# Performance work log

Measured on AMD Instinct MI355X. Metric: run time of the kernel, lower is better.

Reference implementation:

```python
import jax, jax.numpy as jnp
import numpy as np

T = 8          # message-passing steps (hparams['T'])
D = 64         # link_state_dim
R = 128        # readout_units
E = 100000     # num edges (rows of link_state)
M = 400000     # num messages (len of states_first/second)
G = 1000       # num graphs in the batch


def _gru_cell(x, h, W, U, b):
    """Keras GRUCell with reset_after=True. x:[N,in], h:[N,units].
    W:[in,3u], U:[u,3u], b:[2,3u] (input bias, recurrent bias)."""
    mx = x @ W + b[0]
    mh = h @ U + b[1]
    xz, xr, xh = jnp.split(mx, 3, axis=-1)
    hz, hr, hh = jnp.split(mh, 3, axis=-1)
    z = jax.nn.sigmoid(xz + hz)
    r = jax.nn.sigmoid(xr + hr)
    cand = jnp.tanh(xh + r * hh)
    return z * h + (1.0 - z) * cand


def setup_inputs() -> dict:
    key = jax.random.key(0)
    ks = jax.random.split(key, 12)
    glorot = jax.nn.initializers.glorot_uniform()
    inp = {
        "link_state": jax.random.normal(ks[0], (E, D), jnp.float32),
        "states_first": jax.random.randint(ks[1], (M,), 0, E, jnp.int32),
        "states_second": jax.random.randint(ks[2], (M,), 0, E, jnp.int32),
        "states_graph_ids": jnp.sort(jax.random.randint(ks[3], (E,), 0, G, jnp.int32)),
        "num_edges": E,
        # Message MLP: Dense(D) with selu on concat [*, 2D]
        "W_msg": glorot(ks[4], (2 * D, D), jnp.float32),
        "b_msg": jnp.zeros((D,), jnp.float32),
        # Update GRUCell (units=D, input dim=D)
        "W_upd": glorot(ks[5], (D, 3 * D), jnp.float32),
        "U_upd": glorot(ks[6], (D, 3 * D), jnp.float32),
        "b_upd": jnp.zeros((2, 3 * D), jnp.float32),
        # Readout GRU (units=R, input dim=D)
        "W_ro": glorot(ks[7], (D, 3 * R), jnp.float32),
        "U_ro": glorot(ks[8], (R, 3 * R), jnp.float32),
        "b_ro": jnp.zeros((2, 3 * R), jnp.float32),
        # Final Dense(1)
        "W_out": glorot(ks[9], (R, 1), jnp.float32),
        "b_out": jnp.zeros((1,), jnp.float32),
    }
    return inp


def reference(link_state, states_first, states_second, states_graph_ids, num_edges,
              W_msg, b_msg, W_upd, U_upd, b_upd, W_ro, U_ro, b_ro, W_out, b_out):
    def mp_step(h, _):
        # gather sender/receiver states, concat -> message MLP (selu)
        edges_concat = jnp.concatenate([h[states_first], h[states_second]], axis=1)  # [M, 2D]
        msg = jax.nn.selu(edges_concat @ W_msg + b_msg)                              # [M, D]
        # scatter-add messages to receiver edges
        agg = jax.ops.segment_sum(msg, states_second, num_segments=num_edges)        # [E, D]
        h_new = _gru_cell(agg, h, W_upd, U_upd, b_upd)                               # [E, D]
        return h_new, h_new

    _, seq = jax.lax.scan(mp_step, link_state, None, length=T)  # seq: [T, E, D]

    # Readout GRU over the T-step state sequence per edge; return last hidden state
    def ro_step(h, x_t):
        h_new = _gru_cell(x_t, h, W_ro, U_ro, b_ro)
        return h_new, None

    h0 = jnp.zeros((link_state.shape[0], R), link_state.dtype)
    historial, _ = jax.lax.scan(ro_step, h0, seq)               # [E, R]

    # sorted segment_sum over graph ids, then Dense(1)
    per_graph = jax.ops.segment_sum(historial, states_graph_ids, num_segments=G,
                                    indices_are_sorted=True)    # [G, R]
    return per_graph @ W_out + b_out                             # [G, 1]
```

## Files before the change

kernel.cpp:

```cpp
#include <hip/hip_runtime.h>
#include <hip/hip_bf16.h>

#define D 64
#define R 128
#define NSTEPS 8
#define SELU_SCALE 1.0507009873554805f
#define SELU_ALPHA 1.6732632423543772f
#define PADH 72

typedef _Float16 half8 __attribute__((ext_vector_type(8)));
typedef float f32x4 __attribute__((ext_vector_type(4)));

__device__ __forceinline__ float fast_sig(float x) {
    return __fdividef(1.0f, 1.0f + __expf(-x));
}
__device__ __forceinline__ float fast_tanh(float x) {
    float xc = fminf(fmaxf(x, -15.0f), 15.0f);
    float e = __expf(2.0f * xc);
    return 1.0f - __fdividef(2.0f, e + 1.0f);
}

__global__ __launch_bounds__(256) void swizzle_all(
    const float* __restrict__ Wm, const float* __restrict__ Wu,
    const float* __restrict__ Uu, const float* __restrict__ Wr,
    const float* __restrict__ Ur,
    _Float16* __restrict__ wWm, _Float16* __restrict__ wWu,
    _Float16* __restrict__ wUu, _Float16* __restrict__ wWr,
    _Float16* __restrict__ wUr)
{
    const float* src; _Float16* dst; int K, N;
    switch (blockIdx.y) {
        case 0: src = Wm; dst = wWm; K = 128; N = 64;  break;
        case 1: src = Wu; dst = wWu; K = 64;  N = 192; break;
        case 2: src = Uu; dst = wUu; K = 64;  N = 192; break;
        case 3: src = Wr; dst = wWr; K = 64;  N = 384; break;
        default: src = Ur; dst = wUr; K = 128; N = 384; break;
    }
    int idx = blockIdx.x * 256 + threadIdx.x;
    int KT = K >> 5;
    int total = KT * (N >> 4) * 512;
    if (idx >= total) return;
    int j = idx & 7;
    int lane = (idx >> 3) & 63;
    int kt = (idx >> 9) % KT;
    int nt = idx / (512 * KT);
    int k = 32 * kt + 8 * (lane >> 4) + j;
    int n = 16 * nt + (lane & 15);
    dst[idx] = (_Float16)src[(size_t)k * N + n];
}

__global__ __launch_bounds__(256) void h16_init(const float* __restrict__ src,
                                                _Float16* __restrict__ dst, int n) {
    int i = blockIdx.x * 256 + threadIdx.x;
    if (i < n) dst[i] = (_Float16)src[i];
}

__global__ __launch_bounds__(256) void hist_kernel(const int* __restrict__ second,
                                                   int* __restrict__ cnt, int M) {
    int m = blockIdx.x * 256 + threadIdx.x;
    if (m < M) atomicAdd(&cnt[second[m]], 1);
}

__global__ __launch_bounds__(256) void scan_bsum(const int* __restrict__ cnt,
                                                 int* __restrict__ bsum, int E) {
    int i = blockIdx.x * 256 + threadIdx.x;
    int tid = threadIdx.x;
    int v = (i < E) ? cnt[i] : 0;
    __shared__ int s[256];
    s[tid] = v;
    __syncthreads();
    #pragma unroll
    for (int d = 1; d < 256; d <<= 1) {
        int t = (tid >= d) ? s[tid - d] : 0;
        __syncthreads();
        s[tid] += t;
        __syncthreads();
    }
    if (tid == 255) bsum[blockIdx.x] = s[255];
}

__global__ __launch_bounds__(1024) void scan_part(int* __restrict__ bsum, int NB) {
    int tid = threadIdx.x;
    __shared__ int s[1024];
    int v = (tid < NB) ? bsum[tid] : 0;
    s[tid] = v;
    __syncthreads();
    #pragma unroll
    for (int d = 1; d < 1024; d <<= 1) {
        int t = (tid >= d) ? s[tid - d] : 0;
        __syncthreads();
        s[tid] += t;
        __syncthreads();
    }
    if (tid < NB) bsum[tid] = s[tid] - v;
}

__global__ __launch_bounds__(256) void scan_final(const int* __restrict__ cnt,
                                                  const int* __restrict__ bsum,
                                                  int* __restrict__ off, int E) {
    int i = blockIdx.x * 256 + threadIdx.x;
    int tid = threadIdx.x;
    int v = (i < E) ? cnt[i] : 0;
    __shared__ int s[256];
    s[tid] = v;
    __syncthreads();
    #pragma unroll
    for (int d = 1; d < 256; d <<= 1) {
        int t = (tid >= d) ? s[tid - d] : 0;
        __syncthreads();
        s[tid] += t;
        __syncthreads();
    }
    if (i < E) off[i] = bsum[blockIdx.x] + s[tid] - v;
}

__global__ __launch_bounds__(256) void scatter_kernel(const int* __restrict__ second,
                                                      const int* __restrict__ off,
                                                      int* __restrict__ cur,
                                                      int* __restrict__ perm, int M) {
    int m = blockIdx.x * 256 + threadIdx.x;
    if (m < M) {
        int s = second[m];
        int p = atomicAdd(&cur[s], 1);
        perm[off[s] + p] = m;
    }
}

__global__ __launch_bounds__(256) void fs_pack(const int* __restrict__ first,
                                               const int* __restrict__ second,
                                               const int* __restrict__ perm,
                                               int2* __restrict__ fs, int M) {
    int m = blockIdx.x * 256 + threadIdx.x;
    if (m < M) {
        int pm = perm[m];
        fs[m] = make_int2(first[pm], second[pm]);
    }
}

__global__ __launch_bounds__(256) void step_fused(
    const _Float16* __restrict__ hin,
    _Float16* __restrict__ hout,
    _Float16* hro,
    const int2* __restrict__ fs,
    const int* __restrict__ off,
    const half8* __restrict__ wBm,
    const float* __restrict__ bm,
    const half8* __restrict__ wWu,
    const half8* __restrict__ wUu,
    const float* __restrict__ bu,
    const half8* __restrict__ wWr,
    const half8* __restrict__ wUr,
    const float* __restrict__ br,
    int E, int M)
{
    __shared__ _Float16 smem[4][2][16 * PADH];
    __shared__ int skeys[4][16];

    const int wid = threadIdx.x >> 6;
    const int lane = threadIdx.x & 63;
    const int hi = lane >> 4;
    const int l15 = lane & 15;
    const int e0 = (blockIdx.x * 4 + wid) * 16;

    _Float16* stageH = smem[wid][0];
    _Float16* aggH = smem[wid][1];
    int* skey = skeys[wid];

    {
        unsigned int* az = (unsigned int*)aggH;
        #pragma unroll
        for (int i = 0; i < 9; ++i) az[i * 64 + lane] = 0u;
    }

    half8 Bm[4][4];
    #pragma unroll
    for (int nt = 0; nt < 4; ++nt)
        #pragma unroll
        for (int kt = 0; kt < 4; ++kt)
            Bm[nt][kt] = wBm[(nt * 4 + kt) * 64 + lane];

    if (e0 < E) {
        int b = min(e0 + 16, E);
        int mstart = off[e0];
        int mend = (b == E) ? M : off[b];

        #pragma unroll 1
        for (int ch = 0; mstart + ch * 16 < mend; ++ch) {
            int mrow = mstart + ch * 16 + l15;
            bool mv = (mrow < mend);
            int mcl = min(mrow, mend - 1);
            int2 p = fs[mcl];
            const half8* fr = reinterpret_cast<const half8*>(hin + (size_t)p.x * D);
            const half8* sr = reinterpret_cast<const half8*>(hin + (size_t)p.y * D);
            half8 A[4];
            A[0] = fr[hi];
            A[1] = fr[4 + hi];
            A[2] = sr[hi];
            A[3] = sr[4 + hi];

            f32x4 acc[4];
            #pragma unroll
            for (int nt = 0; nt < 4; ++nt) acc[nt] = (f32x4){0.f, 0.f, 0.f, 0.f};
            #pragma unroll
            for (int nt = 0; nt < 4; ++nt)
                #pragma unroll
                for (int kt = 0; kt < 4; ++kt)
                    acc[nt] = __builtin_amdgcn_mfma_f32_16x16x32_f16(A[kt], Bm[nt][kt], acc[nt], 0, 0, 0);

            #pragma unroll
            for (int nt = 0; nt < 4; ++nt) {
                int n = nt * 16 + l15;
                float bias = bm[n];
                #pragma unroll
                for (int r = 0; r < 4; ++r) {
                    float v = acc[nt][r] + bias;
                    v = (v > 0.0f) ? (SELU_SCALE * v)
                                   : (SELU_SCALE * SELU_ALPHA) * (__expf(v) - 1.0f);
                    stageH[(hi * 4 + r) * PADH + n] = (_Float16)v;
                }
            }
            if (lane < 16) skey[lane] = mv ? (p.y - e0) : -1;

            _Float16 run = (_Float16)0.0f;
            int kprev = skey[0];
            #pragma unroll
            for (int m = 0; m < 16; ++m) {
                int km = skey[m];
                if (km != kprev) {
                    if (kprev >= 0) aggH[kprev * PADH + lane] += run;
                    run = (_Float16)0.0f;
                    kprev = km;
                }
                run += stageH[m * PADH + lane];
            }
            if (kprev >= 0) aggH[kprev * PADH + lane] += run;
        }
    }

    const int ec = min(e0 + l15, E - 1);

    half8 AX[2], AHu[2], AHro[4];
    #pragma unroll
    for (int kt = 0; kt < 2; ++kt) {
        AX[kt] = *reinterpret_cast<const half8*>(&aggH[l15 * PADH + 32 * kt + 8 * hi]);
        AHu[kt] = reinterpret_cast<const half8*>(hin + (size_t)ec * D)[4 * kt + hi];
    }
    #pragma unroll
    for (int kt = 0; kt < 4; ++kt)
        AHro[kt] = reinterpret_cast<const half8*>(hro + (size_t)ec * R)[4 * kt + hi];

    #pragma unroll 1
    for (int i = 0; i < 4; ++i) {
        half8 WBz[2], WBr[2], WBc[2], UBz[2], UBr[2], UBc[2];
        #pragma unroll
        for (int kt = 0; kt < 2; ++kt) {
            WBz[kt] = wWu[((0 + i) * 2 + kt) * 64 + lane];
            WBr[kt] = wWu[((4 + i) * 2 + kt) * 64 + lane];
            WBc[kt] = wWu[((8 + i) * 2 + kt) * 64 + lane];
            UBz[kt] = wUu[((0 + i) * 2 + kt) * 64 + lane];
            UBr[kt] = wUu[((4 + i) * 2 + kt) * 64 + lane];
            UBc[kt] = wUu[((8 + i) * 2 + kt) * 64 + lane];
        }
        int n = 16 * i + l15;
        float bz  = bu[n] + bu[192 + n];
        float brr = bu[64 + n] + bu[256 + n];
        float bx  = bu[128 + n];
        float bh  = bu[320 + n];

        f32x4 az  = (f32x4){0.f, 0.f, 0.f, 0.f};
        f32x4 ar_ = (f32x4){0.f, 0.f, 0.f, 0.f};
        f32x4 acx = (f32x4){0.f, 0.f, 0.f, 0.f};
        f32x4 ach = (f32x4){0.f, 0.f, 0.f, 0.f};
        #pragma unroll
        for (int kt = 0; kt < 2; ++kt) {
            az  = __builtin_amdgcn_mfma_f32_16x16x32_f16(AX[kt], WBz[kt], az, 0, 0, 0);
            az  = __builtin_amdgcn_mfma_f32_16x16x32_f16(AHu[kt], UBz[kt], az, 0, 0, 0);
            ar_ = __builtin_amdgcn_mfma_f32_16x16x32_f16(AX[kt], WBr[kt], ar_, 0, 0, 0);
            ar_ = __builtin_amdgcn_mfma_f32_16x16x32_f16(AHu[kt], UBr[kt], ar_, 0, 0, 0);
            acx = __builtin_amdgcn_mfma_f32_16x16x32_f16(AX[kt], WBc[kt], acx, 0, 0, 0);
            ach = __builtin_amdgcn_mfma_f32_16x16x32_f16(AHu[kt], UBc[kt], ach, 0, 0, 0);
        }
        #pragma unroll
        for (int r = 0; r < 4; ++r) {
            int e = e0 + hi * 4 + r;
            int ecl = min(e, E - 1);
            float z = fast_sig(az[r] + bz);
            float rr = fast_sig(ar_[r] + brr);
            float c = fast_tanh(acx[r] + bx + rr * (ach[r] + bh));
            float hp = (float)hin[(size_t)ecl * D + n];
            float hn = z * hp + (1.0f - z) * c;
            _Float16 hn16 = (_Float16)hn;
            aggH[(hi * 4 + r) * PADH + n] = hn16;
            if (e < E) hout[(size_t)e * D + n] = hn16;
        }
    }

    half8 AXn[2];
    #pragma unroll
    for (int kt = 0; kt < 2; ++kt)
        AXn[kt] = *reinterpret_cast<const half8*>(&aggH[l15 * PADH + 32 * kt + 8 * hi]);

    #pragma unroll 1
    for (int it = 0; it < 8; ++it) {
        half8 WBz[2], WBr[2], WBx[2], UBz[4], UBr[4], UBh[4];
        #pragma unroll
        for (int kt = 0; kt < 2; ++kt) {
            WBz[kt] = wWr[((0 + it) * 2 + kt) * 64 + lane];
            WBr[kt] = wWr[((8 + it) * 2 + kt) * 64 + lane];
            WBx[kt] = wWr[((16 + it) * 2 + kt) * 64 + lane];
        }
        #pragma unroll
        for (int kt = 0; kt < 4; ++kt) {
            UBz[kt] = wUr[((0 + it) * 4 + kt) * 64 + lane];
            UBr[kt] = wUr[((8 + it) * 4 + kt) * 64 + lane];
            UBh[kt] = wUr[((16 + it) * 4 + kt) * 64 + lane];
        }
        int c = it * 16 + l15;
        float bz  = br[c] + br[384 + c];
        float brr = br[128 + c] + br[512 + c];
        float bx  = br[256 + c];
        float bh  = br[640 + c];

        f32x4 az  = (f32x4){0.f, 0.f, 0.f, 0.f};
        f32x4 ar_ = (f32x4){0.f, 0.f, 0.f, 0.f};
        f32x4 acx = (f32x4){0.f, 0.f, 0.f, 0.f};
        f32x4 ach = (f32x4){0.f, 0.f, 0.f, 0.f};
        #pragma unroll
        for (int kt = 0; kt < 2; ++kt) {
            az  = __builtin_amdgcn_mfma_f32_16x16x32_f16(AXn[kt], WBz[kt], az, 0, 0, 0);
            ar_ = __builtin_amdgcn_mfma_f32_16x16x32_f16(AXn[kt], WBr[kt], ar_, 0, 0, 0);
            acx = __builtin_amdgcn_mfma_f32_16x16x32_f16(AXn[kt], WBx[kt], acx, 0, 0, 0);
        }
        #pragma unroll
        for (int kt = 0; kt < 4; ++kt) {
            az  = __builtin_amdgcn_mfma_f32_16x16x32_f16(AHro[kt], UBz[kt], az, 0, 0, 0);
            ar_ = __builtin_amdgcn_mfma_f32_16x16x32_f16(AHro[kt], UBr[kt], ar_, 0, 0, 0);
            ach = __builtin_amdgcn_mfma_f32_16x16x32_f16(AHro[kt], UBh[kt], ach, 0, 0, 0);
        }
        #pragma unroll
        for (int r = 0; r < 4; ++r) {
            int e = e0 + hi * 4 + r;
            int ecl = min(e, E - 1);
            float z = fast_sig(az[r] + bz);
            float rr = fast_sig(ar_[r] + brr);
            float cc = fast_tanh(acx[r] + bx + rr * (ach[r] + bh));
            float hp = (float)hro[(size_t)ecl * R + c];
            if (e < E) hro[(size_t)e * R + c] = (_Float16)(z * hp + (1.0f - z) * cc);
        }
    }
}

__global__ void out_init_kernel(float* __restrict__ out, const float* __restrict__ b_out, int G) {
    int g = blockIdx.x * blockDim.x + threadIdx.x;
    if (g < G) out[g] = b_out[0];
}

__global__ __launch_bounds__(256) void out_kernel(
    const _Float16* __restrict__ hro,
    const int* __restrict__ gid,
    const float* __restrict__ Wout,
    float* __restrict__ out,
    int E)
{
    int e = blockIdx.x * 256 + threadIdx.x;
    int lane = threadIdx.x & 63;
    int ec = min(e, E - 1);
    const half8* hp = reinterpret_cast<const half8*>(hro + (size_t)ec * R);
    float s = 0.0f;
    #pragma unroll
    for (int kk = 0; kk < R / 8; ++kk) {
        half8 v = hp[kk];
        #pragma unroll
        for (int j = 0; j < 8; ++j)
            s = fmaf((float)v[j], Wout[kk * 8 + j], s);
    }
    bool valid = (e < E);
    if (!valid) s = 0.0f;
    int g = valid ? gid[ec] : -1;
    #pragma unroll
    for (int d = 1; d < 64; d <<= 1) {
        float t = __shfl_up(s, d);
        int kg = __shfl_up(g, d);
        if (lane >= d && kg == g) s += t;
    }
    int gnext = __shfl_down(g, 1);
    bool tail = (lane == 63) || (gnext != g);
    if (tail && valid) unsafeAtomicAdd(out + g, s);
}

extern "C" void kernel_launch(void* const* d_in, const int* in_sizes, int n_in,
                              void* d_out, int out_size, void* d_ws, size_t ws_size,
                              hipStream_t stream) {
    const float* link_state = (const float*)d_in[0];
    const int*   first      = (const int*)d_in[1];
    const int*   second     = (const int*)d_in[2];
    const int*   gids       = (const int*)d_in[3];
    const float* Wm         = (const float*)d_in[5];
    const float* bm         = (const float*)d_in[6];
    const float* Wu         = (const float*)d_in[7];
    const float* Uu         = (const float*)d_in[8];
    const float* bu         = (const float*)d_in[9];
    const float* Wr         = (const float*)d_in[10];
    const float* Ur         = (const float*)d_in[11];
    const float* brb        = (const float*)d_in[12];
    const float* Wout       = (const float*)d_in[13];
    const float* bout       = (const float*)d_in[14];

    const int E = in_sizes[0] / D;
    const int M = in_sizes[1];
    const int G = out_size;

    char* p = (char*)d_ws;
    auto carve = [&](size_t bytes) {
        void* r = (void*)p;
        p += (bytes + 255) & ~(size_t)255;
        return r;
    };
    _Float16*  hA   = (_Float16*)carve((size_t)E * D * 2);
    _Float16*  hB   = (_Float16*)carve((size_t)E * D * 2);
    _Float16*  hro  = (_Float16*)carve((size_t)E * R * 2);
    int*       perm = (int*)carve((size_t)M * 4);
    int2*      fs   = (int2*)carve((size_t)M * 8);
    int*       cnt  = (int*)carve((size_t)E * 4);
    int*       cur  = (int*)carve((size_t)E * 4);
    int*       off  = (int*)carve((size_t)(E + 1) * 4);
    int*       bsum = (int*)carve(4096 * 4);
    _Float16*  wWm  = (_Float16*)carve(8192 * 2);
    _Float16*  wWu  = (_Float16*)carve(12288 * 2);
    _Float16*  wUu  = (_Float16*)carve(12288 * 2);
    _Float16*  wWr  = (_Float16*)carve(24576 * 2);
    _Float16*  wUr  = (_Float16*)carve(49152 * 2);

    hipMemsetAsync(hro, 0, (size_t)E * R * 2, stream);
    hipMemsetAsync(cnt, 0, (size_t)E * 4, stream);
    hipMemsetAsync(cur, 0, (size_t)E * 4, stream);

    h16_init<<<(E * D + 255) / 256, 256, 0, stream>>>(link_state, hA, E * D);
    swizzle_all<<<dim3(192, 5), 256, 0, stream>>>(Wm, Wu, Uu, Wr, Ur,
                                                  wWm, wWu, wUu, wWr, wUr);

    const int NB = (E + 255) / 256;
    hist_kernel<<<(M + 255) / 256, 256, 0, stream>>>(second, cnt, M);
    scan_bsum<<<NB, 256, 0, stream>>>(cnt, bsum, E);
    scan_part<<<1, 1024, 0, stream>>>(bsum, NB);
    scan_final<<<NB, 256, 0, stream>>>(cnt, bsum, off, E);
    scatter_kernel<<<(M + 255) / 256, 256, 0, stream>>>(second, off, cur, perm, M);
    fs_pack<<<(M + 255) / 256, 256, 0, stream>>>(first, second, perm, fs, M);

    const int e_blocks = (E + 63) / 64;

    _Float16* hin = hA;
    _Float16* hout = hB;
    for (int t = 0; t < NSTEPS; ++t) {
        step_fused<<<e_blocks, 256, 0, stream>>>(hin, hout, hro, fs, off,
                                                 (const half8*)wWm, bm,
                                                 (const half8*)wWu, (const half8*)wUu, bu,
                                                 (const half8*)wWr, (const half8*)wUr, brb,
                                                 E, M);
        _Float16* tmp = hin; hin = hout; hout = tmp;
    }

    out_init_kernel<<<(G + 255) / 256, 256, 0, stream>>>((float*)d_out, bout, G);
    out_kernel<<<(E + 255) / 256, 256, 0, stream>>>(hro, gids, Wout, (float*)d_out, E);
}
```

Baseline: 851.3 us.

## Replace per-step launches with persistent cooperative kernel keeping readout state in registers

```diff
diff --git a/kernel.cpp b/kernel.cpp
--- a/kernel.cpp
+++ b/kernel.cpp
@@ -1,5 +1,8 @@
 #include <hip/hip_runtime.h>
 #include <hip/hip_bf16.h>
+#include <hip/hip_cooperative_groups.h>
+
+namespace cg = cooperative_groups;
 
 #define D 64
 #define R 128
@@ -7,6 +10,7 @@
 #define SELU_SCALE 1.0507009873554805f
 #define SELU_ALPHA 1.6732632423543772f
 #define PADH 72
+#define PADR 136
 
 typedef _Float16 half8 __attribute__((ext_vector_type(8)));
 typedef float f32x4 __attribute__((ext_vector_type(4)));
@@ -55,6 +59,21 @@
     if (i < n) dst[i] = (_Float16)src[i];
 }
 
+__global__ __launch_bounds__(192) void bias_pack(const float* __restrict__ bu,
+                                                 const float* __restrict__ brr,
+                                                 float4* __restrict__ biasU,
+                                                 float4* __restrict__ biasR) {
+    int c = threadIdx.x;
+    if (c < 64) {
+        biasU[c] = make_float4(bu[c] + bu[192 + c], bu[64 + c] + bu[256 + c],
+                               bu[128 + c], bu[320 + c]);
+    } else {
+        int cr = c - 64;
+        biasR[cr] = make_float4(brr[cr] + brr[384 + cr], brr[128 + cr] + brr[512 + cr],
+                                brr[256 + cr], brr[640 + cr]);
+    }
+}
+
 __global__ __launch_bounds__(256) void hist_kernel(const int* __restrict__ second,
                                                    int* __restrict__ cnt, int M) {
     int m = blockIdx.x * 256 + threadIdx.x;
@@ -134,6 +153,295 @@
     if (m < M) {
         int pm = perm[m];
         fs[m] = make_int2(first[pm], second[pm]);
+    }
+}
+
+__device__ __forceinline__ void step_group(
+    int e0, bool last,
+    const _Float16* __restrict__ hin, _Float16* __restrict__ hout,
+    _Float16* __restrict__ hro,
+    const int2* __restrict__ fs, const int* __restrict__ off,
+    const half8 (&Bm)[4][4], const float* __restrict__ bm,
+    const half8* __restrict__ wWu, const half8* __restrict__ wUu,
+    const float4* __restrict__ biasU,
+    const half8* __restrict__ wWr, const half8* __restrict__ wUr,
+    const float4* __restrict__ biasR,
+    _Float16* stageH, _Float16* aggH, _Float16* rotile, int* skey,
+    half8& hpC0, half8& hpC1, half8& hpC2, half8& hpC3,
+    int E, int M, int lane, int hi, int l15)
+{
+    {
+        unsigned int* az = (unsigned int*)aggH;
+        #pragma unroll
+        for (int i = 0; i < 9; ++i) az[i * 64 + lane] = 0u;
+    }
+
+    if (e0 < E) {
+        int b = min(e0 + 16, E);
+        int mstart = off[e0];
+        int mend = (b == E) ? M : off[b];
+
+        #pragma unroll 1
+        for (int chk = 0; mstart + chk * 16 < mend; ++chk) {
+            int mrow = mstart + chk * 16 + l15;
+            bool mv = (mrow < mend);
+            int mcl = min(mrow, mend - 1);
+            int2 p = fs[mcl];
+            const half8* fr = reinterpret_cast<const half8*>(hin + (size_t)p.x * D);
+            const half8* sr = reinterpret_cast<const half8*>(hin + (size_t)p.y * D);
+            half8 A[4];
+            A[0] = fr[hi];
+            A[1] = fr[4 + hi];
+            A[2] = sr[hi];
+            A[3] = sr[4 + hi];
+
+            f32x4 acc[4];
+            #pragma unroll
+            for (int nt = 0; nt < 4; ++nt) acc[nt] = (f32x4){0.f, 0.f, 0.f, 0.f};
+            #pragma unroll
+            for (int nt = 0; nt < 4; ++nt)
+                #pragma unroll
+                for (int kt = 0; kt < 4; ++kt)
+                    acc[nt] = __builtin_amdgcn_mfma_f32_16x16x32_f16(A[kt], Bm[nt][kt], acc[nt], 0, 0, 0);
+
+            #pragma unroll
+            for (int nt = 0; nt < 4; ++nt) {
+                int n = nt * 16 + l15;
+                float bias = bm[n];
+                #pragma unroll
+                for (int r = 0; r < 4; ++r) {
+                    float v = acc[nt][r] + bias;
+                    v = (v > 0.0f) ? (SELU_SCALE * v)
+                                   : (SELU_SCALE * SELU_ALPHA) * (__expf(v) - 1.0f);
+                    stageH[(hi * 4 + r) * PADH + n] = (_Float16)v;
+                }
+            }
+            if (lane < 16) skey[lane] = mv ? (p.y - e0) : -1;
+
+            _Float16 run = (_Float16)0.0f;
+            int kprev = skey[0];
+            #pragma unroll
+            for (int m = 0; m < 16; ++m) {
+                int km = skey[m];
+                if (km != kprev) {
+                    if (kprev >= 0) aggH[kprev * PADH + lane] += run;
+                    run = (_Float16)0.0f;
+                    kprev = km;
+                }
+                run += stageH[m * PADH + lane];
+            }
+            if (kprev >= 0) aggH[kprev * PADH + lane] += run;
+        }
+    }
+
+    const int ec = min(e0 + l15, E - 1);
+
+    half8 AX[2], AHu[2];
+    #pragma unroll
+    for (int kt = 0; kt < 2; ++kt) {
+        AX[kt] = *reinterpret_cast<const half8*>(&aggH[l15 * PADH + 32 * kt + 8 * hi]);
+        AHu[kt] = reinterpret_cast<const half8*>(hin + (size_t)ec * D)[4 * kt + hi];
+    }
+
+    #pragma unroll 1
+    for (int i = 0; i < 4; ++i) {
+        half8 WBz[2], WBr[2], WBc[2], UBz[2], UBr[2], UBc[2];
+        #pragma unroll
+        for (int kt = 0; kt < 2; ++kt) {
+            WBz[kt] = wWu[((0 + i) * 2 + kt) * 64 + lane];
+            WBr[kt] = wWu[((4 + i) * 2 + kt) * 64 + lane];
+            WBc[kt] = wWu[((8 + i) * 2 + kt) * 64 + lane];
+            UBz[kt] = wUu[((0 + i) * 2 + kt) * 64 + lane];
+            UBr[kt] = wUu[((4 + i) * 2 + kt) * 64 + lane];
+            UBc[kt] = wUu[((8 + i) * 2 + kt) * 64 + lane];
+        }
+        int n = 16 * i + l15;
+        float4 bU = biasU[n];
+
+        f32x4 az  = (f32x4){0.f, 0.f, 0.f, 0.f};
+        f32x4 ar_ = (f32x4){0.f, 0.f, 0.f, 0.f};
+        f32x4 acx = (f32x4){0.f, 0.f, 0.f, 0.f};
+        f32x4 ach = (f32x4){0.f, 0.f, 0.f, 0.f};
+        #pragma unroll
+        for (int kt = 0; kt < 2; ++kt) {
+            az  = __builtin_amdgcn_mfma_f32_16x16x32_f16(AX[kt], WBz[kt], az, 0, 0, 0);
+            az  = __builtin_amdgcn_mfma_f32_16x16x32_f16(AHu[kt], UBz[kt], az, 0, 0, 0);
+            ar_ = __builtin_amdgcn_mfma_f32_16x16x32_f16(AX[kt], WBr[kt], ar_, 0, 0, 0);
+            ar_ = __builtin_amdgcn_mfma_f32_16x16x32_f16(AHu[kt], UBr[kt], ar_, 0, 0, 0);
+            acx = __builtin_amdgcn_mfma_f32_16x16x32_f16(AX[kt], WBc[kt], acx, 0, 0, 0);
+            ach = __builtin_amdgcn_mfma_f32_16x16x32_f16(AHu[kt], UBc[kt], ach, 0, 0, 0);
+        }
+        #pragma unroll
+        for (int r = 0; r < 4; ++r) {
+            int e = e0 + hi * 4 + r;
+            int ecl = min(e, E - 1);
+            float z = fast_sig(az[r] + bU.x);
+            float rr = fast_sig(ar_[r] + bU.y);
+            float c = fast_tanh(acx[r] + bU.z + rr * (ach[r] + bU.w));
+            float hp = (float)hin[(size_t)ecl * D + n];
+            float hn = z * hp + (1.0f - z) * c;
+            _Float16 hn16 = (_Float16)hn;
+            aggH[(hi * 4 + r) * PADH + n] = hn16;
+            if (!last && e < E) hout[(size_t)e * D + n] = hn16;
+        }
+    }
+
+    half8 AXn[2];
+    #pragma unroll
+    for (int kt = 0; kt < 2; ++kt)
+        AXn[kt] = *reinterpret_cast<const half8*>(&aggH[l15 * PADH + 32 * kt + 8 * hi]);
+
+    #pragma unroll 1
+    for (int q = 0; q < 4; ++q) {
+        half8 cur;
+        switch (q) {
+            case 0: cur = hpC0; break;
+            case 1: cur = hpC1; break;
+            case 2: cur = hpC2; break;
+            default: cur = hpC3; break;
+        }
+        #pragma unroll
+        for (int jj = 0; jj < 8; ++jj) {
+            int it = 2 * q + (jj >> 2);
+            int r = jj & 3;
+            rotile[(hi * 4 + r) * PADR + it * 16 + l15] = cur[jj];
+        }
+    }
+    half8 AHro[4];
+    #pragma unroll
+    for (int kt = 0; kt < 4; ++kt)
+        AHro[kt] = *reinterpret_cast<const half8*>(&rotile[l15 * PADR + 32 * kt + 8 * hi]);
+
+    #pragma unroll 1
+    for (int q = 0; q < 4; ++q) {
+        half8 cur;
+        switch (q) {
+            case 0: cur = hpC0; break;
+            case 1: cur = hpC1; break;
+            case 2: cur = hpC2; break;
+            default: cur = hpC3; break;
+        }
+        half8 nxt;
+        #pragma unroll
+        for (int par = 0; par < 2; ++par) {
+            int it = 2 * q + par;
+            half8 WBz[2], WBr[2], WBx[2], UBz[4], UBr[4], UBh[4];
+            #pragma unroll
+            for (int kt = 0; kt < 2; ++kt) {
+                WBz[kt] = wWr[((0 + it) * 2 + kt) * 64 + lane];
+                WBr[kt] = wWr[((8 + it) * 2 + kt) * 64 + lane];
+                WBx[kt] = wWr[((16 + it) * 2 + kt) * 64 + lane];
+            }
+            #pragma unroll
+            for (int kt = 0; kt < 4; ++kt) {
+                UBz[kt] = wUr[((0 + it) * 4 + kt) * 64 + lane];
+                UBr[kt] = wUr[((8 + it) * 4 + kt) * 64 + lane];
+                UBh[kt] = wUr[((16 + it) * 4 + kt) * 64 + lane];
+            }
+            int c = it * 16 + l15;
+            float4 bR = biasR[c];
+
+            f32x4 az  = (f32x4){0.f, 0.f, 0.f, 0.f};
+            f32x4 ar_ = (f32x4){0.f, 0.f, 0.f, 0.f};
+            f32x4 acx = (f32x4){0.f, 0.f, 0.f, 0.f};
+            f32x4 ach = (f32x4){0.f, 0.f, 0.f, 0.f};
+            #pragma unroll
+            for (int kt = 0; kt < 2; ++kt) {
+                az  = __builtin_amdgcn_mfma_f32_16x16x32_f16(AXn[kt], WBz[kt], az, 0, 0, 0);
+                ar_ = __builtin_amdgcn_mfma_f32_16x16x32_f16(AXn[kt], WBr[kt], ar_, 0, 0, 0);
+                acx = __builtin_amdgcn_mfma_f32_16x16x32_f16(AXn[kt], WBx[kt], acx, 0, 0, 0);
+            }
+            #pragma unroll
+            for (int kt = 0; kt < 4; ++kt) {
+                az  = __builtin_amdgcn_mfma_f32_16x16x32_f16(AHro[kt], UBz[kt], az, 0, 0, 0);
+                ar_ = __builtin_amdgcn_mfma_f32_16x16x32_f16(AHro[kt], UBr[kt], ar_, 0, 0, 0);
+                ach = __builtin_amdgcn_mfma_f32_16x16x32_f16(AHro[kt], UBh[kt], ach, 0, 0, 0);
+            }
+            #pragma unroll
+            for (int r = 0; r < 4; ++r) {
+                int e = e0 + hi * 4 + r;
+                float z = fast_sig(az[r] + bR.x);
+                float rr = fast_sig(ar_[r] + bR.y);
+                float cc = fast_tanh(acx[r] + bR.z + rr * (ach[r] + bR.w));
+                float hp = (float)cur[par * 4 + r];
+                float hn = z * hp + (1.0f - z) * cc;
+                _Float16 hn16 = (_Float16)hn;
+                nxt[par * 4 + r] = hn16;
+                if (last && e < E) hro[(size_t)e * R + c] = hn16;
+            }
+        }
+        switch (q) {
+            case 0: hpC0 = nxt; break;
+            case 1: hpC1 = nxt; break;
+            case 2: hpC2 = nxt; break;
+            default: hpC3 = nxt; break;
+        }
+    }
+}
+
+__global__ __launch_bounds__(256, 4) void mp_persistent(
+    _Float16* hA, _Float16* hB,
+    _Float16* __restrict__ hro,
+    const int2* __restrict__ fs,
+    const int* __restrict__ off,
+    const half8* __restrict__ wBm,
+    const float* __restrict__ bm,
+    const half8* __restrict__ wWu, const half8* __restrict__ wUu,
+    const float4* __restrict__ biasU,
+    const half8* __restrict__ wWr, const half8* __restrict__ wUr,
+    const float4* __restrict__ biasR,
+    int E, int M, int ngroups)
+{
+    cg::grid_group grid = cg::this_grid();
+
+    __shared__ _Float16 region[4][2304];
+    __shared__ int skeys[4][16];
+
+    const int wid = threadIdx.x >> 6;
+    const int lane = threadIdx.x & 63;
+    const int hi = lane >> 4;
+    const int l15 = lane & 15;
+
+    _Float16* stageH = &region[wid][0];
+    _Float16* aggH = &region[wid][1152];
+    _Float16* rotile = &region[wid][0];
+    int* skey = skeys[wid];
+
+    half8 Bm[4][4];
+    #pragma unroll
+    for (int nt = 0; nt < 4; ++nt)
+        #pragma unroll
+        for (int kt = 0; kt < 4; ++kt)
+            Bm[nt][kt] = wBm[(nt * 4 + kt) * 64 + lane];
+
+    half8 hpA0 = {}, hpA1 = {}, hpA2 = {}, hpA3 = {};
+    half8 hpB0 = {}, hpB1 = {}, hpB2 = {}, hpB3 = {};
+
+    const int grpA = blockIdx.x;
+    const int grpB = blockIdx.x + gridDim.x;
+
+    const _Float16* hin = hA;
+    _Float16* hout = hB;
+
+    #pragma unroll 1
+    for (int t = 0; t < NSTEPS; ++t) {
+        const bool last = (t == NSTEPS - 1);
+
+        if (grpA < ngroups)
+            step_group(grpA * 64 + wid * 16, last, hin, hout, hro, fs, off,
+                       Bm, bm, wWu, wUu, biasU, wWr, wUr, biasR,
+                       stageH, aggH, rotile, skey,
+                       hpA0, hpA1, hpA2, hpA3, E, M, lane, hi, l15);
+        if (grpB < ngroups)
+            step_group(grpB * 64 + wid * 16, last, hin, hout, hro, fs, off,
+                       Bm, bm, wWu, wUu, biasU, wWr, wUr, biasR,
+                       stageH, aggH, rotile, skey,
+                       hpB0, hpB1, hpB2, hpB3, E, M, lane, hi, l15);
+
+        if (!last) {
+            grid.sync();
+            const _Float16* tp = hin; hin = hout; hout = (_Float16*)tp;
+        }
     }
 }
 
@@ -416,20 +724,22 @@
         p += (bytes + 255) & ~(size_t)255;
         return r;
     };
-    _Float16*  hA   = (_Float16*)carve((size_t)E * D * 2);
-    _Float16*  hB   = (_Float16*)carve((size_t)E * D * 2);
-    _Float16*  hro  = (_Float16*)carve((size_t)E * R * 2);
-    int*       perm = (int*)carve((size_t)M * 4);
-    int2*      fs   = (int2*)carve((size_t)M * 8);
-    int*       cnt  = (int*)carve((size_t)E * 4);
-    int*       cur  = (int*)carve((size_t)E * 4);
-    int*       off  = (int*)carve((size_t)(E + 1) * 4);
-    int*       bsum = (int*)carve(4096 * 4);
-    _Float16*  wWm  = (_Float16*)carve(8192 * 2);
-    _Float16*  wWu  = (_Float16*)carve(12288 * 2);
-    _Float16*  wUu  = (_Float16*)carve(12288 * 2);
-    _Float16*  wWr  = (_Float16*)carve(24576 * 2);
-    _Float16*  wUr  = (_Float16*)carve(49152 * 2);
+    _Float16*  hA    = (_Float16*)carve((size_t)E * D * 2);
+    _Float16*  hB    = (_Float16*)carve((size_t)E * D * 2);
+    _Float16*  hro   = (_Float16*)carve((size_t)E * R * 2);
+    int*       perm  = (int*)carve((size_t)M * 4);
+    int2*      fs    = (int2*)carve((size_t)M * 8);
+    int*       cnt   = (int*)carve((size_t)E * 4);
+    int*       cur   = (int*)carve((size_t)E * 4);
+    int*       off   = (int*)carve((size_t)(E + 1) * 4);
+    int*       bsum  = (int*)carve(4096 * 4);
+    _Float16*  wWm   = (_Float16*)carve(8192 * 2);
+    _Float16*  wWu   = (_Float16*)carve(12288 * 2);
+    _Float16*  wUu   = (_Float16*)carve(12288 * 2);
+    _Float16*  wWr   = (_Float16*)carve(24576 * 2);
+    _Float16*  wUr   = (_Float16*)carve(49152 * 2);
+    float4*    biasU = (float4*)carve(64 * 16);
+    float4*    biasR = (float4*)carve(128 * 16);
 
     hipMemsetAsync(hro, 0, (size_t)E * R * 2, stream);
     hipMemsetAsync(cnt, 0, (size_t)E * 4, stream);
@@ -438,6 +748,7 @@
     h16_init<<<(E * D + 255) / 256, 256, 0, stream>>>(link_state, hA, E * D);
     swizzle_all<<<dim3(192, 5), 256, 0, stream>>>(Wm, Wu, Uu, Wr, Ur,
                                                   wWm, wWu, wUu, wWr, wUr);
+    bias_pack<<<1, 192, 0, stream>>>(bu, brb, biasU, biasR);
 
     const int NB = (E + 255) / 256;
     hist_kernel<<<(M + 255) / 256, 256, 0, stream>>>(second, cnt, M);
@@ -447,17 +758,39 @@
     scatter_kernel<<<(M + 255) / 256, 256, 0, stream>>>(second, off, cur, perm, M);
     fs_pack<<<(M + 255) / 256, 256, 0, stream>>>(first, second, perm, fs, M);
 
-    const int e_blocks = (E + 63) / 64;
-
-    _Float16* hin = hA;
-    _Float16* hout = hB;
-    for (int t = 0; t < NSTEPS; ++t) {
-        step_fused<<<e_blocks, 256, 0, stream>>>(hin, hout, hro, fs, off,
-                                                 (const half8*)wWm, bm,
-                                                 (const half8*)wWu, (const half8*)wUu, bu,
-                                                 (const half8*)wWr, (const half8*)wUr, brb,
-                                                 E, M);
-        _Float16* tmp = hin; hin = hout; hout = tmp;
+    const int ngroups = (E + 63) / 64;
+
+    int maxb = 0;
+    hipOccupancyMaxActiveBlocksPerMultiprocessor(&maxb, mp_persistent, 256, 0);
+    int dev = 0, nCU = 0;
+    hipGetDevice(&dev);
+    hipDeviceGetAttribute(&nCU, hipDeviceAttributeMultiprocessorCount, dev);
+    long capacity = (long)maxb * (long)nCU;
+
+    if (capacity > 0 && capacity * 2 >= (long)ngroups) {
+        int blocks = (int)((capacity < (long)ngroups) ? capacity : (long)ngroups);
+        int E_ = E, M_ = M, ng_ = ngroups;
+        void* kargs[] = {
+            (void*)&hA, (void*)&hB, (void*)&hro, (void*)&fs, (void*)&off,
+            (void*)&wWm, (void*)&bm,
+            (void*)&wWu, (void*)&wUu, (void*)&biasU,
+            (void*)&wWr, (void*)&wUr, (void*)&biasR,
+            (void*)&E_, (void*)&M_, (void*)&ng_
+        };
+        hipLaunchCooperativeKernel((const void*)mp_persistent, dim3(blocks), dim3(256),
+                                   kargs, 0, stream);
+    } else {
+        const int e_blocks = ngroups;
+        _Float16* hin = hA;
+        _Float16* hout = hB;
+        for (int t = 0; t < NSTEPS; ++t) {
+            step_fused<<<e_blocks, 256, 0, stream>>>(hin, hout, hro, fs, off,
+                                                     (const half8*)wWm, bm,
+                                                     (const half8*)wWu, (const half8*)wUu, bu,
+                                                     (const half8*)wWr, (const half8*)wUr, brb,
+                                                     E, M);
+            _Float16* tmp = hin; hin = hout; hout = tmp;
+        }
     }
 
     out_init_kernel<<<(G + 255) / 256, 256, 0, stream>>>((float*)d_out, bout, G);
```

Measured after the change: 859.8 us. About the same (+1.0%).

## Split readout GRU into one kernel keeping its hidden state in registers

Applied to the files above, without the earlier changes.

```diff
diff --git a/kernel.cpp b/kernel.cpp
--- a/kernel.cpp
+++ b/kernel.cpp
@@ -7,6 +7,7 @@
 #define SELU_SCALE 1.0507009873554805f
 #define SELU_ALPHA 1.6732632423543772f
 #define PADH 72
+#define PADR 136
 
 typedef _Float16 half8 __attribute__((ext_vector_type(8)));
 typedef float f32x4 __attribute__((ext_vector_type(4)));
@@ -55,6 +56,21 @@
     if (i < n) dst[i] = (_Float16)src[i];
 }
 
+__global__ __launch_bounds__(192) void bias_pack(const float* __restrict__ bu,
+                                                 const float* __restrict__ brr,
+                                                 float4* __restrict__ biasU,
+                                                 float4* __restrict__ biasR) {
+    int c = threadIdx.x;
+    if (c < 64) {
+        biasU[c] = make_float4(bu[c] + bu[192 + c], bu[64 + c] + bu[256 + c],
+                               bu[128 + c], bu[320 + c]);
+    } else {
+        int cr = c - 64;
+        biasR[cr] = make_float4(brr[cr] + brr[384 + cr], brr[128 + cr] + brr[512 + cr],
+                                brr[256 + cr], brr[640 + cr]);
+    }
+}
+
 __global__ __launch_bounds__(256) void hist_kernel(const int* __restrict__ second,
                                                    int* __restrict__ cnt, int M) {
     int m = blockIdx.x * 256 + threadIdx.x;
@@ -137,20 +153,16 @@
     }
 }
 
-__global__ __launch_bounds__(256) void step_fused(
+__global__ __launch_bounds__(256) void msg_upd(
     const _Float16* __restrict__ hin,
     _Float16* __restrict__ hout,
-    _Float16* hro,
     const int2* __restrict__ fs,
     const int* __restrict__ off,
     const half8* __restrict__ wBm,
     const float* __restrict__ bm,
     const half8* __restrict__ wWu,
     const half8* __restrict__ wUu,
-    const float* __restrict__ bu,
-    const half8* __restrict__ wWr,
-    const half8* __restrict__ wUr,
-    const float* __restrict__ br,
+    const float4* __restrict__ biasU,
     int E, int M)
 {
     __shared__ _Float16 smem[4][2][16 * PADH];
@@ -179,7 +191,9 @@
         for (int kt = 0; kt < 4; ++kt)
             Bm[nt][kt] = wBm[(nt * 4 + kt) * 64 + lane];
 
-    if (e0 < E) {
+    if (e0 >= E) return;
+
+    {
         int b = min(e0 + 16, E);
         int mstart = off[e0];
         int mend = (b == E) ? M : off[b];
@@ -239,15 +253,12 @@
 
     const int ec = min(e0 + l15, E - 1);
 
-    half8 AX[2], AHu[2], AHro[4];
+    half8 AX[2], AHu[2];
     #pragma unroll
     for (int kt = 0; kt < 2; ++kt) {
         AX[kt] = *reinterpret_cast<const half8*>(&aggH[l15 * PADH + 32 * kt + 8 * hi]);
         AHu[kt] = reinterpret_cast<const half8*>(hin + (size_t)ec * D)[4 * kt + hi];
     }
-    #pragma unroll
-    for (int kt = 0; kt < 4; ++kt)
-        AHro[kt] = reinterpret_cast<const half8*>(hro + (size_t)ec * R)[4 * kt + hi];
 
     #pragma unroll 1
     for (int i = 0; i < 4; ++i) {
@@ -262,10 +273,7 @@
             UBc[kt] = wUu[((8 + i) * 2 + kt) * 64 + lane];
         }
         int n = 16 * i + l15;
-        float bz  = bu[n] + bu[192 + n];
-        float brr = bu[64 + n] + bu[256 + n];
-        float bx  = bu[128 + n];
-        float bh  = bu[320 + n];
+        float4 bU = biasU[n];
 
         f32x4 az  = (f32x4){0.f, 0.f, 0.f, 0.f};
         f32x4 ar_ = (f32x4){0.f, 0.f, 0.f, 0.f};
@@ -284,68 +292,166 @@
         for (int r = 0; r < 4; ++r) {
             int e = e0 + hi * 4 + r;
             int ecl = min(e, E - 1);
-            float z = fast_sig(az[r] + bz);
-            float rr = fast_sig(ar_[r] + brr);
-            float c = fast_tanh(acx[r] + bx + rr * (ach[r] + bh));
+            float z = fast_sig(az[r] + bU.x);
+            float rr = fast_sig(ar_[r] + bU.y);
+            float c = fast_tanh(acx[r] + bU.z + rr * (ach[r] + bU.w));
             float hp = (float)hin[(size_t)ecl * D + n];
             float hn = z * hp + (1.0f - z) * c;
-            _Float16 hn16 = (_Float16)hn;
-            aggH[(hi * 4 + r) * PADH + n] = hn16;
-            if (e < E) hout[(size_t)e * D + n] = hn16;
-        }
-    }
-
-    half8 AXn[2];
-    #pragma unroll
-    for (int kt = 0; kt < 2; ++kt)
-        AXn[kt] = *reinterpret_cast<const half8*>(&aggH[l15 * PADH + 32 * kt + 8 * hi]);
+            if (e < E) hout[(size_t)e * D + n] = (_Float16)hn;
+        }
+    }
+}
+
+__global__ __launch_bounds__(256) void ro_all(
+    const _Float16* __restrict__ hseq1,
+    const int* __restrict__ gid,
+    const float* __restrict__ Wout,
+    const half8* __restrict__ wWr,
+    const half8* __restrict__ wUr,
+    const float4* __restrict__ biasR,
+    float* __restrict__ out,
+    int E, int edelems)
+{
+    __shared__ _Float16 rotile_s[4][16 * PADR];
+
+    const int wid = threadIdx.x >> 6;
+    const int lane = threadIdx.x & 63;
+    const int hi = lane >> 4;
+    const int l15 = lane & 15;
+    const int e0 = (blockIdx.x * 4 + wid) * 16;
+    if (e0 >= E) return;
+
+    _Float16* rotile = rotile_s[wid];
+    const int ec = min(e0 + l15, E - 1);
+
+    half8 hpC0 = {}, hpC1 = {}, hpC2 = {}, hpC3 = {};
 
     #pragma unroll 1
-    for (int it = 0; it < 8; ++it) {
-        half8 WBz[2], WBr[2], WBx[2], UBz[4], UBr[4], UBh[4];
-        #pragma unroll
-        for (int kt = 0; kt < 2; ++kt) {
-            WBz[kt] = wWr[((0 + it) * 2 + kt) * 64 + lane];
-            WBr[kt] = wWr[((8 + it) * 2 + kt) * 64 + lane];
-            WBx[kt] = wWr[((16 + it) * 2 + kt) * 64 + lane];
-        }
-        #pragma unroll
-        for (int kt = 0; kt < 4; ++kt) {
-            UBz[kt] = wUr[((0 + it) * 4 + kt) * 64 + lane];
-            UBr[kt] = wUr[((8 + it) * 4 + kt) * 64 + lane];
-            UBh[kt] = wUr[((16 + it) * 4 + kt) * 64 + lane];
-        }
-        int c = it * 16 + l15;
-        float bz  = br[c] + br[384 + c];
-        float brr = br[128 + c] + br[512 + c];
-        float bx  = br[256 + c];
-        float bh  = br[640 + c];
-
-        f32x4 az  = (f32x4){0.f, 0.f, 0.f, 0.f};
-        f32x4 ar_ = (f32x4){0.f, 0.f, 0.f, 0.f};
-        f32x4 acx = (f32x4){0.f, 0.f, 0.f, 0.f};
-        f32x4 ach = (f32x4){0.f, 0.f, 0.f, 0.f};
-        #pragma unroll
-        for (int kt = 0; kt < 2; ++kt) {
-            az  = __builtin_amdgcn_mfma_f32_16x16x32_f16(AXn[kt], WBz[kt], az, 0, 0, 0);
-            ar_ = __builtin_amdgcn_mfma_f32_16x16x32_f16(AXn[kt], WBr[kt], ar_, 0, 0, 0);
-            acx = __builtin_amdgcn_mfma_f32_16x16x32_f16(AXn[kt], WBx[kt], acx, 0, 0, 0);
-        }
-        #pragma unroll
-        for (int kt = 0; kt < 4; ++kt) {
-            az  = __builtin_amdgcn_mfma_f32_16x16x32_f16(AHro[kt], UBz[kt], az, 0, 0, 0);
-            ar_ = __builtin_amdgcn_mfma_f32_16x16x32_f16(AHro[kt], UBr[kt], ar_, 0, 0, 0);
-            ach = __builtin_amdgcn_mfma_f32_16x16x32_f16(AHro[kt], UBh[kt], ach, 0, 0, 0);
-        }
+    for (int t = 0; t < NSTEPS; ++t) {
+        const _Float16* ht = hseq1 + (size_t)t * edelems;
+
+        half8 AXt[2];
+        #pragma unroll
+        for (int kt = 0; kt < 2; ++kt)
+            AXt[kt] = reinterpret_cast<const half8*>(ht + (size_t)ec * D)[4 * kt + hi];
+
+        #pragma unroll
+        for (int q = 0; q < 4; ++q) {
+            half8 cur;
+            switch (q) {
+                case 0: cur = hpC0; break;
+                case 1: cur = hpC1; break;
+                case 2: cur = hpC2; break;
+                default: cur = hpC3; break;
+            }
+            #pragma unroll
+            for (int jj = 0; jj < 8; ++jj) {
+                int it = 2 * q + (jj >> 2);
+                int r = jj & 3;
+                rotile[(hi * 4 + r) * PADR + it * 16 + l15] = cur[jj];
+            }
+        }
+        half8 AHro[4];
+        #pragma unroll
+        for (int kt = 0; kt < 4; ++kt)
+            AHro[kt] = *reinterpret_cast<const half8*>(&rotile[l15 * PADR + 32 * kt + 8 * hi]);
+
+        #pragma unroll 1
+        for (int q = 0; q < 4; ++q) {
+            half8 cur;
+            switch (q) {
+                case 0: cur = hpC0; break;
+                case 1: cur = hpC1; break;
+                case 2: cur = hpC2; break;
+                default: cur = hpC3; break;
+            }
+            half8 nxt;
+            #pragma unroll
+            for (int par = 0; par < 2; ++par) {
+                int it = 2 * q + par;
+                half8 WBz[2], WBr[2], WBx[2], UBz[4], UBr[4], UBh[4];
+                #pragma unroll
+                for (int kt = 0; kt < 2; ++kt) {
+                    WBz[kt] = wWr[((0 + it) * 2 + kt) * 64 + lane];
+                    WBr[kt] = wWr[((8 + it) * 2 + kt) * 64 + lane];
+                    WBx[kt] = wWr[((16 + it) * 2 + kt) * 64 + lane];
+                }
+                #pragma unroll
+                for (int kt = 0; kt < 4; ++kt) {
+                    UBz[kt] = wUr[((0 + it) * 4 + kt) * 64 + lane];
+                    UBr[kt] = wUr[((8 + it) * 4 + kt) * 64 + lane];
+                    UBh[kt] = wUr[((16 + it) * 4 + kt) * 64 + lane];
+                }
+                int c = it * 16 + l15;
+                float4 bR = biasR[c];
+
+                f32x4 az  = (f32x4){0.f, 0.f, 0.f, 0.f};
+                f32x4 ar_ = (f32x4){0.f, 0.f, 0.f, 0.f};
+                f32x4 acx = (f32x4){0.f, 0.f, 0.f, 0.f};
+                f32x4 ach = (f32x4){0.f, 0.f, 0.f, 0.f};
+                #pragma unroll
+                for (int kt = 0; kt < 2; ++kt) {
+                    az  = __builtin_amdgcn_mfma_f32_16x16x32_f16(AXt[kt], WBz[kt], az, 0, 0, 0);
+                    ar_ = __builtin_amdgcn_mfma_f32_16x16x32_f16(AXt[kt], WBr[kt], ar_, 0, 0, 0);
+                    acx = __builtin_amdgcn_mfma_f32_16x16x32_f16(AXt[kt], WBx[kt], acx, 0, 0, 0);
+                }
+                #pragma unroll
+                for (int kt = 0; kt < 4; ++kt) {
+                    az  = __builtin_amdgcn_mfma_f32_16x16x32_f16(AHro[kt], UBz[kt], az, 0, 0, 0);
+                    ar_ = __builtin_amdgcn_mfma_f32_16x16x32_f16(AHro[kt], UBr[kt], ar_, 0, 0, 0);
+                    ach = __builtin_amdgcn_mfma_f32_16x16x32_f16(AHro[kt], UBh[kt], ach, 0, 0, 0);
+                }
+                #pragma unroll
+                for (int r = 0; r < 4; ++r) {
+                    float z = fast_sig(az[r] + bR.x);
+                    float rr = fast_sig(ar_[r] + bR.y);
+                    float cc = fast_tanh(acx[r] + bR.z + rr * (ach[r] + bR.w));
+                    float hp = (float)cur[par * 4 + r];
+                    float hn = z * hp + (1.0f - z) * cc;
+                    nxt[par * 4 + r] = (_Float16)hn;
+                }
+            }
+            switch (q) {
+                case 0: hpC0 = nxt; break;
+                case 1: hpC1 = nxt; break;
+                case 2: hpC2 = nxt; break;
+                default: hpC3 = nxt; break;
+            }
+        }
+    }
+
+    float wv[8];
+    #pragma unroll
+    for (int it = 0; it < 8; ++it) wv[it] = Wout[it * 16 + l15];
+
+    float part[4] = {0.f, 0.f, 0.f, 0.f};
+    #pragma unroll
+    for (int q = 0; q < 4; ++q) {
+        half8 cur;
+        switch (q) {
+            case 0: cur = hpC0; break;
+            case 1: cur = hpC1; break;
+            case 2: cur = hpC2; break;
+            default: cur = hpC3; break;
+        }
+        #pragma unroll
+        for (int jj = 0; jj < 8; ++jj) {
+            int it = 2 * q + (jj >> 2);
+            int r = jj & 3;
+            part[r] = fmaf((float)cur[jj], wv[it], part[r]);
+        }
+    }
+    #pragma unroll
+    for (int d = 1; d < 16; d <<= 1) {
+        #pragma unroll
+        for (int r = 0; r < 4; ++r)
+            part[r] += __shfl_xor(part[r], d);
+    }
+    if (l15 == 0) {
         #pragma unroll
         for (int r = 0; r < 4; ++r) {
             int e = e0 + hi * 4 + r;
-            int ecl = min(e, E - 1);
-            float z = fast_sig(az[r] + bz);
-            float rr = fast_sig(ar_[r] + brr);
-            float cc = fast_tanh(acx[r] + bx + rr * (ach[r] + bh));
-            float hp = (float)hro[(size_t)ecl * R + c];
-            if (e < E) hro[(size_t)e * R + c] = (_Float16)(z * hp + (1.0f - z) * cc);
+            if (e < E) unsafeAtomicAdd(out + gid[e], part[r]);
         }
     }
 }
@@ -353,39 +459,6 @@
 __global__ void out_init_kernel(float* __restrict__ out, const float* __restrict__ b_out, int G) {
     int g = blockIdx.x * blockDim.x + threadIdx.x;
     if (g < G) out[g] = b_out[0];
-}
-
-__global__ __launch_bounds__(256) void out_kernel(
-    const _Float16* __restrict__ hro,
-    const int* __restrict__ gid,
-    const float* __restrict__ Wout,
-    float* __restrict__ out,
-    int E)
-{
-    int e = blockIdx.x * 256 + threadIdx.x;
-    int lane = threadIdx.x & 63;
-    int ec = min(e, E - 1);
-    const half8* hp = reinterpret_cast<const half8*>(hro + (size_t)ec * R);
-    float s = 0.0f;
-    #pragma unroll
-    for (int kk = 0; kk < R / 8; ++kk) {
-        half8 v = hp[kk];
-        #pragma unroll
-        for (int j = 0; j < 8; ++j)
-            s = fmaf((float)v[j], Wout[kk * 8 + j], s);
-    }
-    bool valid = (e < E);
-    if (!valid) s = 0.0f;
-    int g = valid ? gid[ec] : -1;
-    #pragma unroll
-    for (int d = 1; d < 64; d <<= 1) {
-        float t = __shfl_up(s, d);
-        int kg = __shfl_up(g, d);
-        if (lane >= d && kg == g) s += t;
-    }
-    int gnext = __shfl_down(g, 1);
-    bool tail = (lane == 63) || (gnext != g);
-    if (tail && valid) unsafeAtomicAdd(out + g, s);
 }
 
 extern "C" void kernel_launch(void* const* d_in, const int* in_sizes, int n_in,
@@ -416,28 +489,29 @@
         p += (bytes + 255) & ~(size_t)255;
         return r;
     };
-    _Float16*  hA   = (_Float16*)carve((size_t)E * D * 2);
-    _Float16*  hB   = (_Float16*)carve((size_t)E * D * 2);
-    _Float16*  hro  = (_Float16*)carve((size_t)E * R * 2);
-    int*       perm = (int*)carve((size_t)M * 4);
-    int2*      fs   = (int2*)carve((size_t)M * 8);
-    int*       cnt  = (int*)carve((size_t)E * 4);
-    int*       cur  = (int*)carve((size_t)E * 4);
-    int*       off  = (int*)carve((size_t)(E + 1) * 4);
-    int*       bsum = (int*)carve(4096 * 4);
-    _Float16*  wWm  = (_Float16*)carve(8192 * 2);
-    _Float16*  wWu  = (_Float16*)carve(12288 * 2);
-    _Float16*  wUu  = (_Float16*)carve(12288 * 2);
-    _Float16*  wWr  = (_Float16*)carve(24576 * 2);
-    _Float16*  wUr  = (_Float16*)carve(49152 * 2);
-
-    hipMemsetAsync(hro, 0, (size_t)E * R * 2, stream);
+    const size_t edelems = (size_t)E * D;
+    _Float16*  hseq  = (_Float16*)carve(edelems * 2 * (NSTEPS + 1));
+    int*       perm  = (int*)carve((size_t)M * 4);
+    int2*      fs    = (int2*)carve((size_t)M * 8);
+    int*       cnt   = (int*)carve((size_t)E * 4);
+    int*       cur   = (int*)carve((size_t)E * 4);
+    int*       off   = (int*)carve((size_t)(E + 1) * 4);
+    int*       bsum  = (int*)carve(4096 * 4);
+    _Float16*  wWm   = (_Float16*)carve(8192 * 2);
+    _Float16*  wWu   = (_Float16*)carve(12288 * 2);
+    _Float16*  wUu   = (_Float16*)carve(12288 * 2);
+    _Float16*  wWr   = (_Float16*)carve(24576 * 2);
+    _Float16*  wUr   = (_Float16*)carve(49152 * 2);
+    float4*    biasU = (float4*)carve(64 * 16);
+    float4*    biasR = (float4*)carve(128 * 16);
+
     hipMemsetAsync(cnt, 0, (size_t)E * 4, stream);
     hipMemsetAsync(cur, 0, (size_t)E * 4, stream);
 
-    h16_init<<<(E * D + 255) / 256, 256, 0, stream>>>(link_state, hA, E * D);
+    h16_init<<<(E * D + 255) / 256, 256, 0, stream>>>(link_state, hseq, E * D);
     swizzle_all<<<dim3(192, 5), 256, 0, stream>>>(Wm, Wu, Uu, Wr, Ur,
                                                   wWm, wWu, wUu, wWr, wUr);
+    bias_pack<<<1, 192, 0, stream>>>(bu, brb, biasU, biasR);
 
     const int NB = (E + 255) / 256;
     hist_kernel<<<(M + 255) / 256, 256, 0, stream>>>(second, cnt, M);
@@ -449,17 +523,17 @@
 
     const int e_blocks = (E + 63) / 64;
 
-    _Float16* hin = hA;
-    _Float16* hout = hB;
     for (int t = 0; t < NSTEPS; ++t) {
-        step_fused<<<e_blocks, 256, 0, stream>>>(hin, hout, hro, fs, off,
-                                                 (const half8*)wWm, bm,
-                                                 (const half8*)wWu, (const half8*)wUu, bu,
-                                                 (const half8*)wWr, (const half8*)wUr, brb,
-                                                 E, M);
-        _Float16* tmp = hin; hin = hout; hout = tmp;
+        msg_upd<<<e_blocks, 256, 0, stream>>>(hseq + (size_t)t * edelems,
+                                              hseq + (size_t)(t + 1) * edelems,
+                                              fs, off,
+                                              (const half8*)wWm, bm,
+                                              (const half8*)wWu, (const half8*)wUu, biasU,
+                                              E, M);
     }
 
     out_init_kernel<<<(G + 255) / 256, 256, 0, stream>>>((float*)d_out, bout, G);
-    out_kernel<<<(E + 255) / 256, 256, 0, stream>>>(hro, gids, Wout, (float*)d_out, E);
-}
+    ro_all<<<e_blocks, 256, 0, stream>>>(hseq + edelems, gids, Wout,
+                                         (const half8*)wWr, (const half8*)wUr, biasR,
+                                         (float*)d_out, E, (int)edelems);
+}
```

Measured after the change: 865.8 us. No clear change (+1.7%).
